# Performance work log

Hardware: AMD Instinct MI355X
Metric: run time of the kernel (lower is better)

## Reference

```python
import jax, jax.numpy as jnp
import numpy as np

HEAD_DIM = 128
SCALE = 1.0 / np.sqrt(HEAD_DIM).astype(np.float32)


def setup_inputs() -> dict:
    key = jax.random.key(0)
    kq, kk, kv = jax.random.split(key, 3)
    B, S, H, KVH, D = 2, 2048, 32, 8, HEAD_DIM
    q = jax.random.normal(kq, (B, S, H, D), dtype=jnp.float32)
    k = jax.random.normal(kk, (B, S, KVH, D), dtype=jnp.float32)
    v = jax.random.normal(kv, (B, S, KVH, D), dtype=jnp.float32)
    return {"q": q, "k": k, "v": v}


def reference(q, k, v):
    # q: [B,S,H,D]; k,v: [B,S,KVH,D]
    B, S, H, D = q.shape
    kvh = k.shape[2]
    if kvh != H:
        rep = H // kvh
        # repeat_interleave along head dim (GQA -> MHA expansion)
        k = jnp.repeat(k, rep, axis=2)
        v = jnp.repeat(v, rep, axis=2)
    # scores: [B,H,S,S]
    scores = jnp.einsum("bqhd,bkhd->bhqk", q, k) * SCALE
    causal_mask = jnp.triu(jnp.ones((S, S), dtype=bool), k=1)
    scores = jnp.where(causal_mask, -jnp.inf, scores)
    attn = jax.nn.softmax(scores, axis=-1)
    # output back to [B,S,H,D]
    out = jnp.einsum("bhqk,bkhd->bqhd", attn, v)
    return out
```

## Files before the change

### kernel.cpp

```cpp
#include <hip/hip_runtime.h>
#include <hip/hip_bf16.h>
#include <stdint.h>

#define B_    2
#define S_    2048
#define H_    32
#define KVH_  8
#define D_    128
#define NBLK  256
#define NTOT_ 34

typedef __bf16 bf16x8 __attribute__((ext_vector_type(8)));
typedef unsigned short u16x8 __attribute__((ext_vector_type(8)));
typedef unsigned int u32x4 __attribute__((ext_vector_type(4)));
typedef float f32x16 __attribute__((ext_vector_type(16)));

__device__ constexpr float SCALE_LOG2E = 0.08838834764831845f * 1.4426950408889634f;

__device__ __forceinline__ unsigned short f2bf(float f) {
    unsigned int u = __builtin_bit_cast(unsigned int, f);
    u = (u + 0x7FFFu + ((u >> 16) & 1u)) >> 16;
    return (unsigned short)u;
}

__device__ __forceinline__ unsigned int cvt_pk_bf16(float lo, float hi) {
    unsigned int r;
    asm("v_cvt_pk_bf16_f32 %0, %1, %2" : "=v"(r) : "v"(lo), "v"(hi));
    return r;
}

__device__ __forceinline__ void gload16(const unsigned short* gsrc, unsigned short* ldst) {
    __builtin_amdgcn_global_load_lds(
        (const __attribute__((address_space(1))) unsigned int*)gsrc,
        (__attribute__((address_space(3))) unsigned int*)ldst,
        16, 0, 0);
}

__global__ __launch_bounds__(256) void prepass(const float* __restrict__ k,
                                               const float* __restrict__ v,
                                               unsigned short* __restrict__ kbuf,
                                               unsigned short* __restrict__ vbuf) {
    if (blockIdx.x < 2048) {
        int tid = blockIdx.x * 256 + threadIdx.x;
        int l   = tid & 63;
        int ch  = (tid >> 6) & 7;
        int kt  = (tid >> 9) & 63;
        int kvh = (tid >> 15) & 7;
        int b   = (tid >> 18) & 1;
        int s   = kt * 32 + (l & 31);
        int d0  = ch * 16 + (l >> 5) * 8;
        const float* src = k + (((size_t)b * S_ + s) * KVH_ + kvh) * D_ + d0;
        float4 x = ((const float4*)src)[0];
        float4 y = ((const float4*)src)[1];
        u16x8 o;
        o[0] = f2bf(x.x); o[1] = f2bf(x.y); o[2] = f2bf(x.z); o[3] = f2bf(x.w);
        o[4] = f2bf(y.x); o[5] = f2bf(y.y); o[6] = f2bf(y.z); o[7] = f2bf(y.w);
        *(u16x8*)(kbuf + ((size_t)(((b * KVH_ + kvh) * 64 + kt) * 8 + ch) * 512 + l * 8)) = o;
    } else {
        __shared__ float tile[64][132];
        int bid = blockIdx.x - 2048;
        int u   = bid & 31;
        int kvh = (bid >> 5) & 7;
        int b   = bid >> 8;
        int t   = threadIdx.x;

        int s  = t >> 2;
        int cb = (t & 3) * 32;
        const float* src = v + (((size_t)b * S_ + u * 64 + s) * KVH_ + kvh) * D_ + cb;
        #pragma unroll
        for (int i = 0; i < 8; ++i) {
            float4 x = ((const float4*)src)[i];
            tile[s][cb + 4 * i + 0] = x.x; tile[s][cb + 4 * i + 1] = x.y;
            tile[s][cb + 4 * i + 2] = x.z; tile[s][cb + 4 * i + 3] = x.w;
        }
        __syncthreads();

        #pragma unroll
        for (int i = 0; i < 4; ++i) {
            int slot = t + 256 * i;
            int ci = slot >> 6;
            int l  = slot & 63;
            int kk = ci >> 2, dt = ci & 3;
            int h2 = l >> 5;
            u16x8 o;
            #pragma unroll
            for (int j = 0; j < 8; ++j)
                o[j] = f2bf(tile[kk * 16 + h2 * 8 + j][dt * 32 + (l & 31)]);
            *(u16x8*)(vbuf + ((size_t)(((b * KVH_ + kvh) * 32 + u) * 16 + ci) * 512 + l * 8)) = o;
        }
    }
}

__global__ __launch_bounds__(512, 2)
void attn_fwd(const float* __restrict__ q,
              const unsigned short* __restrict__ kbuf,
              const unsigned short* __restrict__ vbuf,
              float* __restrict__ out)
{
    int pid = blockIdx.x;
    int lid = (pid & 7) * (NBLK / 8) + (pid >> 3);
    int p    = lid & 7;
    int hp   = (lid >> 3) & 1;
    int bkvh = lid >> 4;
    int b    = bkvh >> 3, kvh = bkvh & 7;
    const int qtA = 15 - p;
    const int NTA = 2 * qtA + 2;
    const int qtB = p;

    const int tid = threadIdx.x, wave = tid >> 6, lane = tid & 63;
    const int cw = wave & 3;
    const int h  = kvh * 4 + hp * 2 + (wave >> 2);
    const int c32 = lane & 31, hi = lane >> 5;

    __shared__ __align__(16) unsigned short ldsK[2][8192];
    __shared__ __align__(16) unsigned short ldsV[2][8192];

    const unsigned short* kfb = kbuf + (size_t)(b * KVH_ + kvh) * (S_ * D_);
    const unsigned short* vfb = vbuf + (size_t)(b * KVH_ + kvh) * (S_ * D_);

    auto kvt = [&](int u) { return (u < NTA) ? u : (u - NTA); };
    auto stageK = [&](int u) {
        const unsigned short* ks = kfb + (size_t)kvt(u) * 8192;
        unsigned short* ld = &ldsK[u & 1][0];
        #pragma unroll
        for (int i = 0; i < 2; ++i) {
            int seg = wave * 2 + i;
            gload16(ks + seg * 512 + lane * 8, ld + seg * 512);
        }
    };
    auto stageV = [&](int u) {
        const unsigned short* vs = vfb + (size_t)kvt(u) * 8192;
        unsigned short* ld = &ldsV[u & 1][0];
        #pragma unroll
        for (int i = 0; i < 2; ++i) {
            int seg = wave * 2 + i;
            gload16(vs + seg * 512 + lane * 8, ld + seg * 512);
        }
    };

    stageK(0);
    asm volatile("s_waitcnt vmcnt(0)" ::: "memory");
    __builtin_amdgcn_s_barrier();
    asm volatile("" ::: "memory");

    auto run_tile = [&](int qt, int u0, int NT) {
        const int q0w = qt * 128 + cw * 32;

        bf16x8 qf[8];
        {
            const float* qp = q + ((size_t)b * S_ + q0w + c32) * (H_ * D_) + h * D_ + hi * 8;
            #pragma unroll
            for (int ch = 0; ch < 8; ++ch) {
                float4 a  = ((const float4*)(qp + ch * 16))[0];
                float4 bb = ((const float4*)(qp + ch * 16))[1];
                u16x8 tt;
                tt[0] = f2bf(a.x * SCALE_LOG2E);  tt[1] = f2bf(a.y * SCALE_LOG2E);
                tt[2] = f2bf(a.z * SCALE_LOG2E);  tt[3] = f2bf(a.w * SCALE_LOG2E);
                tt[4] = f2bf(bb.x * SCALE_LOG2E); tt[5] = f2bf(bb.y * SCALE_LOG2E);
                tt[6] = f2bf(bb.z * SCALE_LOG2E); tt[7] = f2bf(bb.w * SCALE_LOG2E);
                qf[ch] = __builtin_bit_cast(bf16x8, tt);
            }
        }

        f32x16 acc[4];
        #pragma unroll
        for (int dt = 0; dt < 4; ++dt)
            #pragma unroll
            for (int i = 0; i < 16; ++i) acc[dt][i] = 0.f;
        float lsum = 0.f;

        u32x4 pfA[4], pfB[4];

        auto body = [&](int u, int it, int NT_, u32x4 (&pfW)[4], u32x4 (&pfR)[4], int ODD) {
            if (u + 1 < NTOT_) stageK(u + 1);
            stageV(u);
            const int k0 = it * 64;
            const bool act  = (k0 <= q0w + 31);
            const bool pact = (it > 0) && (k0 - 64 <= q0w + 31);
            f32x16 sv[2];

            if (act) {
                #pragma unroll
                for (int kt = 0; kt < 2; ++kt)
                    #pragma unroll
                    for (int i = 0; i < 16; ++i) sv[kt][i] = 0.f;
                __builtin_amdgcn_s_setprio(1);
                #pragma unroll
                for (int ch = 0; ch < 8; ++ch) {
                    bf16x8 kf0 = *(const bf16x8*)&ldsK[ODD][(0 * 8 + ch) * 512 + lane * 8];
                    bf16x8 kf1 = *(const bf16x8*)&ldsK[ODD][(1 * 8 + ch) * 512 + lane * 8];
                    sv[0] = __builtin_amdgcn_mfma_f32_32x32x16_bf16(kf0, qf[ch], sv[0], 0, 0, 0);
                    sv[1] = __builtin_amdgcn_mfma_f32_32x32x16_bf16(kf1, qf[ch], sv[1], 0, 0, 0);
                }
                __builtin_amdgcn_s_setprio(0);
            }

            if (pact) {
                __builtin_amdgcn_s_setprio(1);
                #pragma unroll
                for (int kk = 0; kk < 4; ++kk) {
                    bf16x8 pb = __builtin_bit_cast(bf16x8, pfR[kk]);
                    #pragma unroll
                    for (int dt = 0; dt < 4; ++dt) {
                        bf16x8 vf = *(const bf16x8*)&ldsV[ODD ^ 1][(kk * 4 + dt) * 512 + lane * 8];
                        acc[dt] = __builtin_amdgcn_mfma_f32_32x32x16_bf16(vf, pb, acc[dt], 0, 0, 0);
                    }
                }
                __builtin_amdgcn_s_setprio(0);
            }

            if (act) {
                if (k0 + 63 > q0w) {
                    #pragma unroll
                    for (int kt = 0; kt < 2; ++kt)
                        #pragma unroll
                        for (int r = 0; r < 16; ++r) {
                            int key = k0 + 32 * kt + (r & 3) + 8 * (r >> 2) + 4 * hi;
                            if (key > q0w + c32) sv[kt][r] = -INFINITY;
                        }
                }

                float pp[2][16];
                float sacc = 0.f;
                #pragma unroll
                for (int kt = 0; kt < 2; ++kt)
                    #pragma unroll
                    for (int r = 0; r < 16; ++r) {
                        pp[kt][r] = exp2f(sv[kt][r]);
                        sacc += pp[kt][r];
                    }
                lsum += sacc;

                #pragma unroll
                for (int kt = 0; kt < 2; ++kt) {
                    #pragma unroll
                    for (int kap = 0; kap < 2; ++kap) {
                        int base = kap * 8;
                        unsigned int U0 = cvt_pk_bf16(pp[kt][base + 0], pp[kt][base + 1]);
                        unsigned int U1 = cvt_pk_bf16(pp[kt][base + 2], pp[kt][base + 3]);
                        unsigned int V0 = cvt_pk_bf16(pp[kt][base + 4], pp[kt][base + 5]);
                        unsigned int V1 = cvt_pk_bf16(pp[kt][base + 6], pp[kt][base + 7]);
                        asm volatile("v_permlane32_swap_b32 %0, %1" : "+v"(U0), "+v"(V0));
                        asm volatile("v_permlane32_swap_b32 %0, %1" : "+v"(U1), "+v"(V1));
                        u32x4 W;
                        W[0] = U0;
                        W[1] = U1;
                        W[2] = V0;
                        W[3] = V1;
                        pfW[kt * 2 + kap] = W;
                    }
                }
            }

            asm volatile("s_waitcnt vmcnt(0)" ::: "memory");
            __builtin_amdgcn_s_barrier();
            asm volatile("" ::: "memory");
        };

        for (int it = 0; it < NT; it += 2) {
            body(u0 + it,     it,     NT, pfA, pfB, 0);
            body(u0 + it + 1, it + 1, NT, pfB, pfA, 1);
        }

        if (cw >= 2) {
            #pragma unroll
            for (int kk = 0; kk < 4; ++kk) {
                bf16x8 pb = __builtin_bit_cast(bf16x8, pfB[kk]);
                #pragma unroll
                for (int dt = 0; dt < 4; ++dt) {
                    bf16x8 vf = *(const bf16x8*)&ldsV[1][(kk * 4 + dt) * 512 + lane * 8];
                    acc[dt] = __builtin_amdgcn_mfma_f32_32x32x16_bf16(vf, pb, acc[dt], 0, 0, 0);
                }
            }
        }

        lsum += __shfl_xor(lsum, 32);
        float linv = 1.0f / lsum;
        float* ob = out + ((size_t)b * S_ + q0w + c32) * (H_ * D_) + h * D_;
        #pragma unroll
        for (int dt = 0; dt < 4; ++dt)
            #pragma unroll
            for (int rq = 0; rq < 4; ++rq) {
                float4 o;
                o.x = acc[dt][4 * rq + 0] * linv;
                o.y = acc[dt][4 * rq + 1] * linv;
                o.z = acc[dt][4 * rq + 2] * linv;
                o.w = acc[dt][4 * rq + 3] * linv;
                *(float4*)(ob + dt * 32 + rq * 8 + hi * 4) = o;
            }
    };

    run_tile(qtA, 0, NTA);
    run_tile(qtB, NTA, NTOT_ - NTA);
}

extern "C" void kernel_launch(void* const* d_in, const int* in_sizes, int n_in,
                              void* d_out, int out_size, void* d_ws, size_t ws_size,
                              hipStream_t stream) {
    const float* q = (const float*)d_in[0];
    const float* k = (const float*)d_in[1];
    const float* v = (const float*)d_in[2];
    float* out = (float*)d_out;

    unsigned short* kbuf = (unsigned short*)d_ws;
    unsigned short* vbuf = kbuf + (size_t)B_ * KVH_ * S_ * D_;

    prepass<<<2560, 256, 0, stream>>>(k, v, kbuf, vbuf);
    attn_fwd<<<NBLK, 512, 0, stream>>>(q, kbuf, vbuf, out);
}
```

Baseline: 112.3 us.

## Split attention blocks per head with 32-key tiles and 4-wave workgroups

Each workgroup now handles a single query head with 4 waves instead of two heads with 8 waves, which doubles the grid to 512 blocks. The key tile shrinks from 64 to 32 keys, so LDS buffers halve and there are twice as many pipeline iterations. The goal is more blocks and waves resident per CU and finer causal granularity. In exchange, K/V reuse across the GQA head pair is lost, so staged memory traffic doubles, and per-iteration barrier overhead doubles.

```diff
diff --git a/kernel.cpp b/kernel.cpp
--- a/kernel.cpp
+++ b/kernel.cpp
@@ -7,8 +7,8 @@
 #define H_    32
 #define KVH_  8
 #define D_    128
-#define NBLK  256
-#define NTOT_ 34
+#define NBLK  512
+#define NTOT_ 68
 
 typedef __bf16 bf16x8 __attribute__((ext_vector_type(8)));
 typedef unsigned short u16x8 __attribute__((ext_vector_type(8)));
@@ -91,7 +91,7 @@
     }
 }
 
-__global__ __launch_bounds__(512, 2)
+__global__ __launch_bounds__(256, 4)
 void attn_fwd(const float* __restrict__ q,
               const unsigned short* __restrict__ kbuf,
               const unsigned short* __restrict__ vbuf,
@@ -99,28 +99,26 @@
 {
     int pid = blockIdx.x;
     int lid = (pid & 7) * (NBLK / 8) + (pid >> 3);
-    int p    = lid & 7;
-    int hp   = (lid >> 3) & 1;
-    int bkvh = lid >> 4;
-    int b    = bkvh >> 3, kvh = bkvh & 7;
+    int p   = lid & 7;
+    int bh  = lid >> 3;
+    int b   = bh >> 5, h = bh & 31, kvh = h >> 2;
     const int qtA = 15 - p;
-    const int NTA = 2 * qtA + 2;
+    const int NTA = 4 * qtA + 4;
     const int qtB = p;
 
     const int tid = threadIdx.x, wave = tid >> 6, lane = tid & 63;
-    const int cw = wave & 3;
-    const int h  = kvh * 4 + hp * 2 + (wave >> 2);
+    const int cw = wave;
     const int c32 = lane & 31, hi = lane >> 5;
 
-    __shared__ __align__(16) unsigned short ldsK[2][8192];
-    __shared__ __align__(16) unsigned short ldsV[2][8192];
+    __shared__ __align__(16) unsigned short ldsK[2][4096];
+    __shared__ __align__(16) unsigned short ldsV[2][4096];
 
     const unsigned short* kfb = kbuf + (size_t)(b * KVH_ + kvh) * (S_ * D_);
     const unsigned short* vfb = vbuf + (size_t)(b * KVH_ + kvh) * (S_ * D_);
 
     auto kvt = [&](int u) { return (u < NTA) ? u : (u - NTA); };
     auto stageK = [&](int u) {
-        const unsigned short* ks = kfb + (size_t)kvt(u) * 8192;
+        const unsigned short* ks = kfb + (size_t)kvt(u) * 4096;
         unsigned short* ld = &ldsK[u & 1][0];
         #pragma unroll
         for (int i = 0; i < 2; ++i) {
@@ -129,7 +127,7 @@
         }
     };
     auto stageV = [&](int u) {
-        const unsigned short* vs = vfb + (size_t)kvt(u) * 8192;
+        const unsigned short* vs = vfb + (size_t)kvt(u) * 4096;
         unsigned short* ld = &ldsV[u & 1][0];
         #pragma unroll
         for (int i = 0; i < 2; ++i) {
@@ -169,28 +167,24 @@
             for (int i = 0; i < 16; ++i) acc[dt][i] = 0.f;
         float lsum = 0.f;
 
-        u32x4 pfA[4], pfB[4];
-
-        auto body = [&](int u, int it, int NT_, u32x4 (&pfW)[4], u32x4 (&pfR)[4], int ODD) {
+        u32x4 pfA[2], pfB[2];
+
+        auto body = [&](int u, int it, u32x4 (&pfW)[2], u32x4 (&pfR)[2], int ODD) {
             if (u + 1 < NTOT_) stageK(u + 1);
             stageV(u);
-            const int k0 = it * 64;
+            const int k0 = it * 32;
             const bool act  = (k0 <= q0w + 31);
-            const bool pact = (it > 0) && (k0 - 64 <= q0w + 31);
-            f32x16 sv[2];
+            const bool pact = (it > 0) && (k0 - 32 <= q0w + 31);
+            f32x16 sv;
 
             if (act) {
                 #pragma unroll
-                for (int kt = 0; kt < 2; ++kt)
-                    #pragma unroll
-                    for (int i = 0; i < 16; ++i) sv[kt][i] = 0.f;
+                for (int i = 0; i < 16; ++i) sv[i] = 0.f;
                 __builtin_amdgcn_s_setprio(1);
                 #pragma unroll
                 for (int ch = 0; ch < 8; ++ch) {
-                    bf16x8 kf0 = *(const bf16x8*)&ldsK[ODD][(0 * 8 + ch) * 512 + lane * 8];
-                    bf16x8 kf1 = *(const bf16x8*)&ldsK[ODD][(1 * 8 + ch) * 512 + lane * 8];
-                    sv[0] = __builtin_amdgcn_mfma_f32_32x32x16_bf16(kf0, qf[ch], sv[0], 0, 0, 0);
-                    sv[1] = __builtin_amdgcn_mfma_f32_32x32x16_bf16(kf1, qf[ch], sv[1], 0, 0, 0);
+                    bf16x8 kf = *(const bf16x8*)&ldsK[ODD][ch * 512 + lane * 8];
+                    sv = __builtin_amdgcn_mfma_f32_32x32x16_bf16(kf, qf[ch], sv, 0, 0, 0);
                 }
                 __builtin_amdgcn_s_setprio(0);
             }
@@ -198,7 +192,7 @@
             if (pact) {
                 __builtin_amdgcn_s_setprio(1);
                 #pragma unroll
-                for (int kk = 0; kk < 4; ++kk) {
+                for (int kk = 0; kk < 2; ++kk) {
                     bf16x8 pb = __builtin_bit_cast(bf16x8, pfR[kk]);
                     #pragma unroll
                     for (int dt = 0; dt < 4; ++dt) {
@@ -210,45 +204,38 @@
             }
 
             if (act) {
-                if (k0 + 63 > q0w) {
-                    #pragma unroll
-                    for (int kt = 0; kt < 2; ++kt)
-                        #pragma unroll
-                        for (int r = 0; r < 16; ++r) {
-                            int key = k0 + 32 * kt + (r & 3) + 8 * (r >> 2) + 4 * hi;
-                            if (key > q0w + c32) sv[kt][r] = -INFINITY;
-                        }
-                }
-
-                float pp[2][16];
-                float sacc = 0.f;
-                #pragma unroll
-                for (int kt = 0; kt < 2; ++kt)
+                if (k0 + 31 > q0w) {
                     #pragma unroll
                     for (int r = 0; r < 16; ++r) {
-                        pp[kt][r] = exp2f(sv[kt][r]);
-                        sacc += pp[kt][r];
+                        int key = k0 + (r & 3) + 8 * (r >> 2) + 4 * hi;
+                        if (key > q0w + c32) sv[r] = -INFINITY;
                     }
-                lsum += sacc;
-
-                #pragma unroll
-                for (int kt = 0; kt < 2; ++kt) {
-                    #pragma unroll
-                    for (int kap = 0; kap < 2; ++kap) {
-                        int base = kap * 8;
-                        unsigned int U0 = cvt_pk_bf16(pp[kt][base + 0], pp[kt][base + 1]);
-                        unsigned int U1 = cvt_pk_bf16(pp[kt][base + 2], pp[kt][base + 3]);
-                        unsigned int V0 = cvt_pk_bf16(pp[kt][base + 4], pp[kt][base + 5]);
-                        unsigned int V1 = cvt_pk_bf16(pp[kt][base + 6], pp[kt][base + 7]);
-                        asm volatile("v_permlane32_swap_b32 %0, %1" : "+v"(U0), "+v"(V0));
-                        asm volatile("v_permlane32_swap_b32 %0, %1" : "+v"(U1), "+v"(V1));
-                        u32x4 W;
-                        W[0] = U0;
-                        W[1] = U1;
-                        W[2] = V0;
-                        W[3] = V1;
-                        pfW[kt * 2 + kap] = W;
-                    }
+                }
+
+                float pp[16];
+                #pragma unroll
+                for (int r = 0; r < 16; ++r) pp[r] = exp2f(sv[r]);
+                float s0 = (pp[0] + pp[1]) + (pp[2] + pp[3]);
+                float s1 = (pp[4] + pp[5]) + (pp[6] + pp[7]);
+                float s2 = (pp[8] + pp[9]) + (pp[10] + pp[11]);
+                float s3 = (pp[12] + pp[13]) + (pp[14] + pp[15]);
+                lsum += (s0 + s1) + (s2 + s3);
+
+                #pragma unroll
+                for (int kap = 0; kap < 2; ++kap) {
+                    int base = kap * 8;
+                    unsigned int U0 = cvt_pk_bf16(pp[base + 0], pp[base + 1]);
+                    unsigned int U1 = cvt_pk_bf16(pp[base + 2], pp[base + 3]);
+                    unsigned int V0 = cvt_pk_bf16(pp[base + 4], pp[base + 5]);
+                    unsigned int V1 = cvt_pk_bf16(pp[base + 6], pp[base + 7]);
+                    asm volatile("v_permlane32_swap_b32 %0, %1" : "+v"(U0), "+v"(V0));
+                    asm volatile("v_permlane32_swap_b32 %0, %1" : "+v"(U1), "+v"(V1));
+                    u32x4 W;
+                    W[0] = U0;
+                    W[1] = U1;
+                    W[2] = V0;
+                    W[3] = V1;
+                    pfW[kap] = W;
                 }
             }
 
@@ -258,13 +245,13 @@
         };
 
         for (int it = 0; it < NT; it += 2) {
-            body(u0 + it,     it,     NT, pfA, pfB, 0);
-            body(u0 + it + 1, it + 1, NT, pfB, pfA, 1);
-        }
-
-        if (cw >= 2) {
-            #pragma unroll
-            for (int kk = 0; kk < 4; ++kk) {
+            body(u0 + it,     it,     pfA, pfB, 0);
+            body(u0 + it + 1, it + 1, pfB, pfA, 1);
+        }
+
+        if (cw == 3) {
+            #pragma unroll
+            for (int kk = 0; kk < 2; ++kk) {
                 bf16x8 pb = __builtin_bit_cast(bf16x8, pfB[kk]);
                 #pragma unroll
                 for (int dt = 0; dt < 4; ++dt) {
@@ -306,5 +293,5 @@
     unsigned short* vbuf = kbuf + (size_t)B_ * KVH_ * S_ * D_;
 
     prepass<<<2560, 256, 0, stream>>>(k, v, kbuf, vbuf);
-    attn_fwd<<<NBLK, 512, 0, stream>>>(q, kbuf, vbuf, out);
-}
+    attn_fwd<<<NBLK, 256, 0, stream>>>(q, kbuf, vbuf, out);
+}
```

Result: slower. 222.3 us (+97.9%).
